# Performance work log

Hardware: AMD Instinct MI355X
Metric: run time of the kernel (lower is better)

Reference implementation:

```python
import jax, jax.numpy as jnp
import numpy as np

DIST_EPS = 0.1   # distance_eps
NORM_EPS = 0.1   # norm_eps
QUAT_EPS = 1e-3
FA_EPS = 1e-5


def normed_vec(V):
    return V / jnp.sqrt((V ** 2).sum(-1, keepdims=True) + NORM_EPS)


def collect_neighbors(node_h, edge_idx):
    # node_h: (B,N,D), edge_idx: (B,N,K) -> (B,N,K,D)
    B, N, K = edge_idx.shape
    D = node_h.shape[-1]
    idx = jnp.broadcast_to(edge_idx.reshape(B, N * K, 1), (B, N * K, D))
    return jnp.take_along_axis(node_h, idx, axis=1).reshape(B, N, K, D)


def field_average(node_h, C, num_fields):
    # per-field mean, scattered back to residues; residues with C==0 get 0
    onehot = (C[..., None] == (jnp.arange(num_fields) + 1)).astype(node_h.dtype)  # (B,N,F)
    sums = jnp.einsum('bnf,bnd->bfd', onehot, node_h)
    counts = jnp.sum(onehot, axis=1)[..., None]  # (B,F,1)
    avg = sums / (counts + FA_EPS)
    return jnp.einsum('bnf,bfd->bnd', onehot, avg)


def reference_frames(X):
    X_N, X_CA, X_C = X[:, :, 0], X[:, :, 1], X[:, :, 2]
    u_CA_N = normed_vec(X_N - X_CA)
    u_CA_C = normed_vec(X_C - X_CA)
    n_1 = u_CA_N
    n_2 = normed_vec(jnp.cross(n_1, u_CA_C))
    n_3 = normed_vec(jnp.cross(n_1, n_2))
    return jnp.stack([n_1, n_2, n_3], -1)  # (B,N,3,3), frames as columns


def reference_frames_field(X, C, num_fields):
    X_N, X_CA, X_C = X[:, :, 0], X[:, :, 1], X[:, :, 2]
    u_CA_N_avg = field_average(normed_vec(X_N - X_CA), C, num_fields)
    u_CA_C_avg = field_average(normed_vec(X_C - X_CA), C, num_fields)
    n_1 = normed_vec(u_CA_N_avg)
    n_2 = normed_vec(jnp.cross(n_1, normed_vec(u_CA_C_avg)))
    n_3 = normed_vec(jnp.cross(n_1, n_2))
    return jnp.stack([n_1, n_2, n_3], -1)


def quaternions_from_rotations(R):
    Rf = R.reshape(R.shape[:-2] + (9,))
    R00, R01, R02, R10, R11, R12, R20, R21, R22 = [Rf[..., i] for i in range(9)]
    mag = 0.5 * jnp.sqrt(jnp.abs(1.0 + jnp.stack([
        R00 + R11 + R22,
        R00 - R11 - R22,
        -R00 + R11 - R22,
        -R00 - R11 + R22], -1)) + QUAT_EPS)
    signs = jnp.sign(jnp.stack([
        jnp.ones_like(R00), R21 - R12, R02 - R20, R10 - R01], -1))
    q = signs * mag
    return q / jnp.sqrt((q ** 2).sum(-1, keepdims=True))


def transformation_features(X_i, X_j, R_i, R_j):
    dX = X_j - X_i[:, :, None]                    # (B,N,K,3)
    L = jnp.sqrt((dX ** 2).sum(-1, keepdims=True) + DIST_EPS)
    u_ij = jnp.einsum('niab,nija->nijb', R_i, dX / L)
    R_rel = jnp.einsum('niab,nijac->nijbc', R_i, R_j)
    q_ij = quaternions_from_rotations(R_rel)
    return jnp.concatenate([jnp.log(L + DIST_EPS), u_ij, q_ij], -1)  # (B,N,K,8)


def setup_inputs() -> dict:
    key = jax.random.key(0)
    k1, k2, k3 = jax.random.split(key, 3)
    B, N, K, NF = 4, 8192, 48, 16
    X = jax.random.normal(k1, (B, N, 4, 3), dtype=jnp.float32)
    edge_idx = jax.random.randint(k2, (B, N, K), 0, N).astype(jnp.int64)
    C = jax.random.randint(k3, (B, N), 0, NF + 1).astype(jnp.int64)
    return {"X": X, "edge_idx": edge_idx, "C": C, "num_fields": NF}


def reference(X, edge_idx, C, num_fields):
    B, N = X.shape[:2]
    R_i = reference_frames(X)
    R_field_i = reference_frames_field(X, C, num_fields)
    X_i = X[:, :, 1, :]  # CA
    X_j = collect_neighbors(X_i, edge_idx)
    X_field_i = field_average(X_i, C, num_fields)
    X_field_j = collect_neighbors(X_field_i, edge_idx)
    R_field_j = collect_neighbors(R_field_i.reshape(B, N, 9), edge_idx).reshape(B, N, -1, 3, 3)
    R_j = collect_neighbors(R_i.reshape(B, N, 9), edge_idx).reshape(B, N, -1, 3, 3)
    h_ff = transformation_features(X_field_i, X_field_j, R_field_i, R_field_j)
    h_fn = transformation_features(X_field_i, X_j, R_field_i, R_j)
    h_nn = transformation_features(X_i, X_j, R_i, R_j)
    edge_h = jnp.concatenate([h_ff, h_fn, h_nn], -1)  # (B,N,K,24)
    mask_i = (C > 0).astype(edge_h.dtype)[..., None]  # (B,N,1)
    mask_j = collect_neighbors(mask_i, edge_idx)      # (B,N,K,1)
    mask_ij = mask_i[:, :, None] * mask_j
    return mask_ij * edge_h
```

## Files before the change

### kernel.cpp

```cpp
#include <hip/hip_runtime.h>
#include <math.h>

#define NFIELDS 16
#define BATCH   4
#define R64_STRIDE 10

#define DIST_EPS 0.1
#define NORM_EPS 0.1
#define QUAT_EPS 0.001
#define FA_EPS   1e-5

#define TAU_NN 1e-4f
#define TAU_FN 1e-5f

#define FS_THREADS 256
__global__ void prep_pass(const float* __restrict__ X, const int* __restrict__ C,
                          double* __restrict__ Rws64, float* __restrict__ nodeF2,
                          double* __restrict__ accum,
                          int N, int BN, int nodeBlocks) {
    __shared__ double red[FS_THREADS][10];
    int t = threadIdx.x;

    if ((int)blockIdx.x < nodeBlocks) {
        int bn = blockIdx.x * blockDim.x + t;
        if (bn >= BN) return;
        const float* xp = X + (size_t)bn * 12;
        double ax = xp[3], ay = xp[4], az = xp[5];

        double ux = (double)xp[0] - ax, uy = (double)xp[1] - ay, uz = (double)xp[2] - az;
        double r1 = 1.0 / sqrt(ux * ux + uy * uy + uz * uz + NORM_EPS);
        ux *= r1; uy *= r1; uz *= r1;

        double vx = (double)xp[6] - ax, vy = (double)xp[7] - ay, vz = (double)xp[8] - az;
        double r2 = 1.0 / sqrt(vx * vx + vy * vy + vz * vz + NORM_EPS);
        vx *= r2; vy *= r2; vz *= r2;

        double wx = uy * vz - uz * vy, wy = uz * vx - ux * vz, wz = ux * vy - uy * vx;
        double r3 = 1.0 / sqrt(wx * wx + wy * wy + wz * wz + NORM_EPS);
        wx *= r3; wy *= r3; wz *= r3;

        double px = uy * wz - uz * wy, py = uz * wx - ux * wz, pz = ux * wy - uy * wx;
        double r4 = 1.0 / sqrt(px * px + py * py + pz * pz + NORM_EPS);
        px *= r4; py *= r4; pz *= r4;

        double* R = Rws64 + (size_t)bn * R64_STRIDE;
        R[0] = ux; R[1] = uy; R[2] = uz;
        R[3] = wx; R[4] = wy; R[5] = wz;
        R[6] = px; R[7] = py; R[8] = pz;

        int c = C[bn];
        float4* nf = (float4*)(nodeF2 + (size_t)bn * 16);
        nf[0] = make_float4((float)ux, (float)uy, (float)uz, (float)wx);
        nf[1] = make_float4((float)wy, (float)wz, (float)px, (float)py);
        nf[2] = make_float4((float)pz, xp[3], xp[4], xp[5]);
        nf[3] = make_float4((float)c, 0.f, 0.f, 0.f);
        return;
    }

    int fb = blockIdx.x - nodeBlocks;
    int b  = fb / NFIELDS;
    int f  = fb % NFIELDS + 1;
    const float* Xb = X + (size_t)b * N * 12;
    const int*   Cb = C + (size_t)b * N;

    double s[10];
#pragma unroll
    for (int i = 0; i < 10; i++) s[i] = 0.0;

    for (int n = t; n < N; n += FS_THREADS) {
        if (Cb[n] == f) {
            const float* xp = Xb + (size_t)n * 12;
            double ax = xp[3], ay = xp[4], az = xp[5];
            double ux = (double)xp[0] - ax, uy = (double)xp[1] - ay, uz = (double)xp[2] - az;
            double r1 = 1.0 / sqrt(ux * ux + uy * uy + uz * uz + NORM_EPS);
            double vx = (double)xp[6] - ax, vy = (double)xp[7] - ay, vz = (double)xp[8] - az;
            double r2 = 1.0 / sqrt(vx * vx + vy * vy + vz * vz + NORM_EPS);
            s[0] += ux * r1; s[1] += uy * r1; s[2] += uz * r1;
            s[3] += vx * r2; s[4] += vy * r2; s[5] += vz * r2;
            s[6] += ax;      s[7] += ay;      s[8] += az;
            s[9] += 1.0;
        }
    }

#pragma unroll
    for (int i = 0; i < 10; i++) red[t][i] = s[i];
    __syncthreads();
    for (int off = FS_THREADS / 2; off > 0; off >>= 1) {
        if (t < off) {
#pragma unroll
            for (int i = 0; i < 10; i++) red[t][i] += red[t + off][i];
        }
        __syncthreads();
    }
    if (t < 10) accum[(size_t)fb * 10 + t] = red[0][t];
}

__device__ __forceinline__ double sgn64(double x) {
    return x > 0.0 ? 1.0 : (x < 0.0 ? -1.0 : 0.0);
}

__device__ __forceinline__ void tf64(double xix, double xiy, double xiz,
                                     double xjx, double xjy, double xjz,
                                     const double* __restrict__ Ri,
                                     const double* __restrict__ Rj,
                                     float* __restrict__ o) {
    double dx = xjx - xix, dy = xjy - xiy, dz = xjz - xiz;
    double L = sqrt(dx * dx + dy * dy + dz * dz + DIST_EPS);
    o[0] = (float)log(L + DIST_EPS);
    double il = 1.0 / L;
    double vx = dx * il, vy = dy * il, vz = dz * il;
    o[1] = (float)(Ri[0] * vx + Ri[1] * vy + Ri[2] * vz);
    o[2] = (float)(Ri[3] * vx + Ri[4] * vy + Ri[5] * vz);
    o[3] = (float)(Ri[6] * vx + Ri[7] * vy + Ri[8] * vz);

    double r00 = Ri[0] * Rj[0] + Ri[1] * Rj[1] + Ri[2] * Rj[2];
    double r01 = Ri[0] * Rj[3] + Ri[1] * Rj[4] + Ri[2] * Rj[5];
    double r02 = Ri[0] * Rj[6] + Ri[1] * Rj[7] + Ri[2] * Rj[8];
    double r10 = Ri[3] * Rj[0] + Ri[4] * Rj[1] + Ri[5] * Rj[2];
    double r11 = Ri[3] * Rj[3] + Ri[4] * Rj[4] + Ri[5] * Rj[5];
    double r12 = Ri[3] * Rj[6] + Ri[4] * Rj[7] + Ri[5] * Rj[8];
    double r20 = Ri[6] * Rj[0] + Ri[7] * Rj[1] + Ri[8] * Rj[2];
    double r21 = Ri[6] * Rj[3] + Ri[7] * Rj[4] + Ri[8] * Rj[5];
    double r22 = Ri[6] * Rj[6] + Ri[7] * Rj[7] + Ri[8] * Rj[8];

    double m0 = 0.5 * sqrt(fabs(1.0 + r00 + r11 + r22) + QUAT_EPS);
    double m1 = 0.5 * sqrt(fabs(1.0 + r00 - r11 - r22) + QUAT_EPS);
    double m2 = 0.5 * sqrt(fabs(1.0 - r00 + r11 - r22) + QUAT_EPS);
    double m3 = 0.5 * sqrt(fabs(1.0 - r00 - r11 + r22) + QUAT_EPS);
    double q0 = m0;
    double q1 = sgn64(r21 - r12) * m1;
    double q2 = sgn64(r02 - r20) * m2;
    double q3 = sgn64(r10 - r01) * m3;
    double qn = 1.0 / sqrt(q0 * q0 + q1 * q1 + q2 * q2 + q3 * q3);
    o[4] = (float)(q0 * qn); o[5] = (float)(q1 * qn);
    o[6] = (float)(q2 * qn); o[7] = (float)(q3 * qn);
}

__global__ void field_finish(const double* __restrict__ accum,
                             double* __restrict__ table64,
                             float* __restrict__ tableF,
                             float* __restrict__ hff) {
    int b = blockIdx.x;
    int t = threadIdx.x;

    if (t <= NFIELDS) {
        double* e = table64 + ((size_t)b * (NFIELDS + 1) + t) * 12;
        float*  eF = tableF + ((size_t)b * (NFIELDS + 1) + t) * 12;
        if (t == 0) {
#pragma unroll
            for (int i = 0; i < 12; i++) { e[i] = 0.0; eF[i] = 0.f; }
        } else {
            const double* s = accum + (size_t)(b * NFIELDS + t - 1) * 10;
            double inv = 1.0 / (s[9] + FA_EPS);
            double axv = s[0] * inv, ayv = s[1] * inv, azv = s[2] * inv;
            double bxv = s[3] * inv, byv = s[4] * inv, bzv = s[5] * inv;
            double xx  = s[6] * inv, xy  = s[7] * inv, xz  = s[8] * inv;

            double r1 = 1.0 / sqrt(axv * axv + ayv * ayv + azv * azv + NORM_EPS);
            double n1x = axv * r1, n1y = ayv * r1, n1z = azv * r1;
            double r2 = 1.0 / sqrt(bxv * bxv + byv * byv + bzv * bzv + NORM_EPS);
            bxv *= r2; byv *= r2; bzv *= r2;

            double wx = n1y * bzv - n1z * byv, wy = n1z * bxv - n1x * bzv, wz = n1x * byv - n1y * bxv;
            double r3 = 1.0 / sqrt(wx * wx + wy * wy + wz * wz + NORM_EPS);
            wx *= r3; wy *= r3; wz *= r3;

            double px = n1y * wz - n1z * wy, py = n1z * wx - n1x * wz, pz = n1x * wy - n1y * wx;
            double r4 = 1.0 / sqrt(px * px + py * py + pz * pz + NORM_EPS);
            px *= r4; py *= r4; pz *= r4;

            e[0] = n1x; e[1] = n1y; e[2] = n1z;
            e[3] = wx;  e[4] = wy;  e[5] = wz;
            e[6] = px;  e[7] = py;  e[8] = pz;
            e[9] = xx;  e[10] = xy; e[11] = xz;
#pragma unroll
            for (int i = 0; i < 12; i++) eF[i] = (float)e[i];
        }
    }
    __syncthreads();

    int ci = t >> 4, cj = t & 15;
    const double* fi = table64 + ((size_t)b * (NFIELDS + 1) + ci + 1) * 12;
    const double* fj = table64 + ((size_t)b * (NFIELDS + 1) + cj + 1) * 12;
    float o[8];
    tf64(fi[9], fi[10], fi[11], fj[9], fj[10], fj[11], fi, fj, o);
    float* hp = hff + (((size_t)b * NFIELDS + ci) * NFIELDS + cj) * 8;
    ((float4*)hp)[0] = make_float4(o[0], o[1], o[2], o[3]);
    ((float4*)hp)[1] = make_float4(o[4], o[5], o[6], o[7]);
}

__device__ __forceinline__ void tf32(float xix, float xiy, float xiz,
                                     float xjx, float xjy, float xjz,
                                     const float* __restrict__ Ri,
                                     const float* __restrict__ Rj,
                                     float s1, float s2, float s3,
                                     float* __restrict__ o) {
    float dx = xjx - xix, dy = xjy - xiy, dz = xjz - xiz;
    float L = sqrtf(dx * dx + dy * dy + dz * dz + 0.1f);
    o[0] = logf(L + 0.1f);
    float il = 1.f / L;
    float vx = dx * il, vy = dy * il, vz = dz * il;
    o[1] = Ri[0] * vx + Ri[1] * vy + Ri[2] * vz;
    o[2] = Ri[3] * vx + Ri[4] * vy + Ri[5] * vz;
    o[3] = Ri[6] * vx + Ri[7] * vy + Ri[8] * vz;

    float r00 = Ri[0] * Rj[0] + Ri[1] * Rj[1] + Ri[2] * Rj[2];
    float r11 = Ri[3] * Rj[3] + Ri[4] * Rj[4] + Ri[5] * Rj[5];
    float r22 = Ri[6] * Rj[6] + Ri[7] * Rj[7] + Ri[8] * Rj[8];

    float m0 = 0.5f * sqrtf(fabsf(1.f + r00 + r11 + r22) + 0.001f);
    float m1 = 0.5f * sqrtf(fabsf(1.f + r00 - r11 - r22) + 0.001f);
    float m2 = 0.5f * sqrtf(fabsf(1.f - r00 + r11 - r22) + 0.001f);
    float m3 = 0.5f * sqrtf(fabsf(1.f - r00 - r11 + r22) + 0.001f);
    float q0 = m0;
    float q1 = s1 * m1;
    float q2 = s2 * m2;
    float q3 = s3 * m3;
    float qn = rsqrtf(q0 * q0 + q1 * q1 + q2 * q2 + q3 * q3);
    o[4] = q0 * qn; o[5] = q1 * qn; o[6] = q2 * qn; o[7] = q3 * qn;
}

__device__ __forceinline__ float fsgn(float x) {
    return x > 0.f ? 1.f : (x < 0.f ? -1.f : 0.f);
}
__device__ __forceinline__ float fsgnd(double x) {
    return x > 0.0 ? 1.f : (x < 0.0 ? -1.f : 0.f);
}
__device__ __forceinline__ int hswz(int idx16) {
    return idx16 ^ ((idx16 >> 3) & 7);
}

__device__ __forceinline__ void edge_core(
        float4 j0, float4 j1, float4 j2, float4 i0, float4 i1, float4 i2,
        const float* __restrict__ tableF, const double* __restrict__ Rws64,
        const double* __restrict__ table64,
        int b, int bn, int bj, int cn, float* __restrict__ o) {
    const float4* ftp = (const float4*)(tableF + ((size_t)b * (NFIELDS + 1) + cn) * 12);
    float4 f0 = ftp[0], f1 = ftp[1], f2 = ftp[2];

    float rj[9] = { j0.x, j0.y, j0.z, j0.w, j1.x, j1.y, j1.z, j1.w, j2.x };
    float cjx = j2.y, cjy = j2.z, cjz = j2.w;
    float ri[9] = { i0.x, i0.y, i0.z, i0.w, i1.x, i1.y, i1.z, i1.w, i2.x };
    float cix = i2.y, ciy = i2.z, ciz = i2.w;
    float fF[9] = { f0.x, f0.y, f0.z, f0.w, f1.x, f1.y, f1.z, f1.w, f2.x };
    float fpx = f2.y, fpy = f2.z, fpz = f2.w;

    float a21 = ri[6]*rj[3] + ri[7]*rj[4] + ri[8]*rj[5] - (ri[3]*rj[6] + ri[4]*rj[7] + ri[5]*rj[8]);
    float a02 = ri[0]*rj[6] + ri[1]*rj[7] + ri[2]*rj[8] - (ri[6]*rj[0] + ri[7]*rj[1] + ri[8]*rj[2]);
    float a10 = ri[3]*rj[0] + ri[4]*rj[1] + ri[5]*rj[2] - (ri[0]*rj[3] + ri[1]*rj[4] + ri[2]*rj[5]);
    float g21 = fF[6]*rj[3] + fF[7]*rj[4] + fF[8]*rj[5] - (fF[3]*rj[6] + fF[4]*rj[7] + fF[5]*rj[8]);
    float g02 = fF[0]*rj[6] + fF[1]*rj[7] + fF[2]*rj[8] - (fF[6]*rj[0] + fF[7]*rj[1] + fF[8]*rj[2]);
    float g10 = fF[3]*rj[0] + fF[4]*rj[1] + fF[5]*rj[2] - (fF[0]*rj[3] + fF[1]*rj[4] + fF[2]*rj[5]);

    float sa21 = fsgn(a21), sa02 = fsgn(a02), sa10 = fsgn(a10);
    float sg21 = fsgn(g21), sg02 = fsgn(g02), sg10 = fsgn(g10);

    float amin = fminf(fminf(fabsf(a21), fabsf(a02)), fabsf(a10));
    float gmin = fminf(fminf(fabsf(g21), fabsf(g02)), fabsf(g10));
    if (amin < TAU_NN || gmin < TAU_FN) {
        const double* RJ = Rws64 + (size_t)bj * R64_STRIDE;
        const double* RI = Rws64 + (size_t)bn * R64_STRIDE;
        const double* FD = table64 + ((size_t)b * (NFIELDS + 1) + cn) * 12;
        double d21 = RI[6]*RJ[3] + RI[7]*RJ[4] + RI[8]*RJ[5] - (RI[3]*RJ[6] + RI[4]*RJ[7] + RI[5]*RJ[8]);
        double d02 = RI[0]*RJ[6] + RI[1]*RJ[7] + RI[2]*RJ[8] - (RI[6]*RJ[0] + RI[7]*RJ[1] + RI[8]*RJ[2]);
        double d10 = RI[3]*RJ[0] + RI[4]*RJ[1] + RI[5]*RJ[2] - (RI[0]*RJ[3] + RI[1]*RJ[4] + RI[2]*RJ[5]);
        double e21 = FD[6]*RJ[3] + FD[7]*RJ[4] + FD[8]*RJ[5] - (FD[3]*RJ[6] + FD[4]*RJ[7] + FD[5]*RJ[8]);
        double e02 = FD[0]*RJ[6] + FD[1]*RJ[7] + FD[2]*RJ[8] - (FD[6]*RJ[0] + FD[7]*RJ[1] + FD[8]*RJ[2]);
        double e10 = FD[3]*RJ[0] + FD[4]*RJ[1] + FD[5]*RJ[2] - (FD[0]*RJ[3] + FD[1]*RJ[4] + FD[2]*RJ[5]);
        sa21 = fsgnd(d21); sa02 = fsgnd(d02); sa10 = fsgnd(d10);
        sg21 = fsgnd(e21); sg02 = fsgnd(e02); sg10 = fsgnd(e10);
    }

    tf32(fpx, fpy, fpz, cjx, cjy, cjz, fF, rj, sg21, sg02, sg10, o + 8);
    tf32(cix, ciy, ciz, cjx, cjy, cjz, ri, rj, sa21, sa02, sa10, o + 16);
}

template <int KC, int NC>
__global__ __launch_bounds__(256)
void edge_pass_lds(const float* __restrict__ nodeF2, const int* __restrict__ eidx,
                   const float* __restrict__ tableF, const float* __restrict__ hff,
                   const double* __restrict__ Rws64, const double* __restrict__ table64,
                   float* __restrict__ out) {
    __shared__ float4 s_hff[2 * NFIELDS * NFIELDS];
    __shared__ float  s_st[128 * 28];

    const int t   = threadIdx.x;
    const int tid = blockIdx.x * 256 + t;
    const int b   = tid / (KC * NC);
    const int bn  = tid / KC;
    const int bj  = b * NC + eidx[tid];

    {
        const float4* src = (const float4*)(hff + (size_t)b * (NFIELDS * NFIELDS * 8));
        s_hff[hswz(t)]       = src[t];
        s_hff[hswz(t + 256)] = src[t + 256];
    }

    const float4* rjp = (const float4*)(nodeF2 + (size_t)bj * 16);
    float4 j0 = rjp[0], j1 = rjp[1], j2 = rjp[2], j3 = rjp[3];
    const float4* rip = (const float4*)(nodeF2 + (size_t)bn * 16);
    float4 i0 = rip[0], i1 = rip[1], i2 = rip[2], i3 = rip[3];

    const int cj = (int)j3.x;
    const int cn = (int)i3.x;
    const bool valid = (cn > 0) && (cj > 0);

    float o[24];
    if (valid) {
        edge_core(j0, j1, j2, i0, i1, i2, tableF, Rws64, table64, b, bn, bj, cn, o);
    } else {
#pragma unroll
        for (int i = 8; i < 24; i++) o[i] = 0.f;
    }

    __syncthreads();
    if (valid) {
        int e = ((cn - 1) * NFIELDS + (cj - 1)) * 2;
        float4 h0 = s_hff[hswz(e)];
        float4 h1 = s_hff[hswz(e + 1)];
        o[0] = h0.x; o[1] = h0.y; o[2] = h0.z; o[3] = h0.w;
        o[4] = h1.x; o[5] = h1.y; o[6] = h1.z; o[7] = h1.w;
    } else {
#pragma unroll
        for (int i = 0; i < 8; i++) o[i] = 0.f;
    }

    float4* outv = (float4*)out + (size_t)blockIdx.x * 1536;

    if (t < 128) {
#pragma unroll
        for (int c = 0; c < 6; c++)
            *(float4*)(s_st + t * 28 + c * 4) =
                make_float4(o[4*c], o[4*c+1], o[4*c+2], o[4*c+3]);
    }
    __syncthreads();
#pragma unroll
    for (int r = 0; r < 3; r++) {
        int f  = t + 256 * r;
        int el = f / 6, c = f - el * 6;
        outv[f] = *(const float4*)(s_st + el * 28 + c * 4);
    }
    __syncthreads();
    if (t >= 128) {
#pragma unroll
        for (int c = 0; c < 6; c++)
            *(float4*)(s_st + (t - 128) * 28 + c * 4) =
                make_float4(o[4*c], o[4*c+1], o[4*c+2], o[4*c+3]);
    }
    __syncthreads();
#pragma unroll
    for (int r = 0; r < 3; r++) {
        int f  = 768 + t + 256 * r;
        int fe = f / 6;
        int el = fe - 128, c = f - fe * 6;
        outv[f] = *(const float4*)(s_st + el * 28 + c * 4);
    }
}

__global__ void edge_pass_gen(const float* __restrict__ nodeF2,
                              const int* __restrict__ eidx,
                              const float* __restrict__ tableF,
                              const float* __restrict__ hff,
                              const double* __restrict__ Rws64,
                              const double* __restrict__ table64,
                              float* __restrict__ out,
                              int N, int K, int total) {
    int tid = blockIdx.x * blockDim.x + threadIdx.x;
    if (tid >= total) return;
    int bn = tid / K;
    int b  = bn / N;
    int bj = b * N + eidx[tid];

    const float4* rjp = (const float4*)(nodeF2 + (size_t)bj * 16);
    float4 j0 = rjp[0], j1 = rjp[1], j2 = rjp[2], j3 = rjp[3];
    const float4* rip = (const float4*)(nodeF2 + (size_t)bn * 16);
    float4 i0 = rip[0], i1 = rip[1], i2 = rip[2], i3 = rip[3];
    int cj = (int)j3.x;
    int cn = (int)i3.x;

    float o[24];
    if (cn > 0 && cj > 0) {
        const float4* hp = (const float4*)(hff +
            (((size_t)b * NFIELDS + (cn - 1)) * NFIELDS + (cj - 1)) * 8);
        float4 h0 = hp[0], h1 = hp[1];
        o[0] = h0.x; o[1] = h0.y; o[2] = h0.z; o[3] = h0.w;
        o[4] = h1.x; o[5] = h1.y; o[6] = h1.z; o[7] = h1.w;
        edge_core(j0, j1, j2, i0, i1, i2, tableF, Rws64, table64, b, bn, bj, cn, o);
    } else {
#pragma unroll
        for (int i = 0; i < 24; i++) o[i] = 0.f;
    }

    float4* op = (float4*)(out + (size_t)tid * 24);
#pragma unroll
    for (int i = 0; i < 6; i++)
        op[i] = make_float4(o[4 * i], o[4 * i + 1], o[4 * i + 2], o[4 * i + 3]);
}

extern "C" void kernel_launch(void* const* d_in, const int* in_sizes, int n_in,
                              void* d_out, int out_size, void* d_ws, size_t ws_size,
                              hipStream_t stream) {
    const float* X  = (const float*)d_in[0];
    const int* eidx = (const int*)d_in[1];
    const int* C    = (const int*)d_in[2];

    const int B  = BATCH;
    const int BN = in_sizes[2];
    const int N  = BN / B;
    const int total = in_sizes[1];
    const int K  = total / BN;

    double* accum   = (double*)d_ws;
    double* table64 = accum + B * NFIELDS * 10;
    double* Rws64   = table64 + B * (NFIELDS + 1) * 12;
    float*  nodeF2  = (float*)(Rws64 + (size_t)BN * R64_STRIDE);
    float*  tableF  = nodeF2 + (size_t)BN * 16;
    float*  hff     = tableF + B * (NFIELDS + 1) * 12;

    int nodeBlocks = (BN + 255) / 256;
    prep_pass<<<nodeBlocks + B * NFIELDS, FS_THREADS, 0, stream>>>(
        X, C, Rws64, nodeF2, accum, N, BN, nodeBlocks);
    field_finish<<<B, 256, 0, stream>>>(accum, table64, tableF, hff);

    if (K == 48 && N == 8192 && (total % 256) == 0) {
        edge_pass_lds<48, 8192><<<total / 256, 256, 0, stream>>>(
            nodeF2, eidx, tableF, hff, Rws64, table64, (float*)d_out);
    } else {
        int eb = (total + 255) / 256;
        edge_pass_gen<<<eb, 256, 0, stream>>>(nodeF2, eidx, tableF, hff,
                                              Rws64, table64, (float*)d_out,
                                              N, K, total);
    }
}
```

Before: 72.85 us.

## Compress node records to 48 bytes, recompute third frame axis, stage field table in LDS

Each per-node record now drops the stored third frame vector and is packed into three float4s instead of four. Edge threads rebuild n3 from n1 and n2 with a cross product and rsqrt, which cuts gather traffic per edge. The per-field frame table is loaded once per block into shared memory instead of being fetched from global per edge. The float-sign fallback thresholds are tightened so the double-precision path triggers less often, trading some sign-robustness margin for fewer slow-path loads, and the recomputed n3 carries a small float error.

```diff
diff --git a/kernel.cpp b/kernel.cpp
--- a/kernel.cpp
+++ b/kernel.cpp
@@ -10,8 +10,8 @@
 #define QUAT_EPS 0.001
 #define FA_EPS   1e-5
 
-#define TAU_NN 1e-4f
-#define TAU_FN 1e-5f
+#define TAU_NN 2e-5f
+#define TAU_FN 2e-6f
 
 #define FS_THREADS 256
 __global__ void prep_pass(const float* __restrict__ X, const int* __restrict__ C,
@@ -51,9 +51,8 @@
         int c = C[bn];
         float4* nf = (float4*)(nodeF2 + (size_t)bn * 16);
         nf[0] = make_float4((float)ux, (float)uy, (float)uz, (float)wx);
-        nf[1] = make_float4((float)wy, (float)wz, (float)px, (float)py);
-        nf[2] = make_float4((float)pz, xp[3], xp[4], xp[5]);
-        nf[3] = make_float4((float)c, 0.f, 0.f, 0.f);
+        nf[1] = make_float4((float)wy, (float)wz, xp[3], xp[4]);
+        nf[2] = make_float4(xp[5], (float)c, 0.f, 0.f);
         return;
     }
 
@@ -229,22 +228,21 @@
 __device__ __forceinline__ int hswz(int idx16) {
     return idx16 ^ ((idx16 >> 3) & 7);
 }
+__device__ __forceinline__ void n3_recompute(const float* __restrict__ r ,
+                                             float* __restrict__ n3) {
+    float px = r[1] * r[5] - r[2] * r[4];
+    float py = r[2] * r[3] - r[0] * r[5];
+    float pz = r[0] * r[4] - r[1] * r[3];
+    float rr = rsqrtf(px * px + py * py + pz * pz + 0.1f);
+    n3[0] = px * rr; n3[1] = py * rr; n3[2] = pz * rr;
+}
 
 __device__ __forceinline__ void edge_core(
-        float4 j0, float4 j1, float4 j2, float4 i0, float4 i1, float4 i2,
-        const float* __restrict__ tableF, const double* __restrict__ Rws64,
-        const double* __restrict__ table64,
+        const float* __restrict__ rj, const float* __restrict__ cjp,
+        const float* __restrict__ ri, const float* __restrict__ cip,
+        const float* __restrict__ fF, const float* __restrict__ fp,
+        const double* __restrict__ Rws64, const double* __restrict__ table64,
         int b, int bn, int bj, int cn, float* __restrict__ o) {
-    const float4* ftp = (const float4*)(tableF + ((size_t)b * (NFIELDS + 1) + cn) * 12);
-    float4 f0 = ftp[0], f1 = ftp[1], f2 = ftp[2];
-
-    float rj[9] = { j0.x, j0.y, j0.z, j0.w, j1.x, j1.y, j1.z, j1.w, j2.x };
-    float cjx = j2.y, cjy = j2.z, cjz = j2.w;
-    float ri[9] = { i0.x, i0.y, i0.z, i0.w, i1.x, i1.y, i1.z, i1.w, i2.x };
-    float cix = i2.y, ciy = i2.z, ciz = i2.w;
-    float fF[9] = { f0.x, f0.y, f0.z, f0.w, f1.x, f1.y, f1.z, f1.w, f2.x };
-    float fpx = f2.y, fpy = f2.z, fpz = f2.w;
-
     float a21 = ri[6]*rj[3] + ri[7]*rj[4] + ri[8]*rj[5] - (ri[3]*rj[6] + ri[4]*rj[7] + ri[5]*rj[8]);
     float a02 = ri[0]*rj[6] + ri[1]*rj[7] + ri[2]*rj[8] - (ri[6]*rj[0] + ri[7]*rj[1] + ri[8]*rj[2]);
     float a10 = ri[3]*rj[0] + ri[4]*rj[1] + ri[5]*rj[2] - (ri[0]*rj[3] + ri[1]*rj[4] + ri[2]*rj[5]);
@@ -271,8 +269,8 @@
         sg21 = fsgnd(e21); sg02 = fsgnd(e02); sg10 = fsgnd(e10);
     }
 
-    tf32(fpx, fpy, fpz, cjx, cjy, cjz, fF, rj, sg21, sg02, sg10, o + 8);
-    tf32(cix, ciy, ciz, cjx, cjy, cjz, ri, rj, sa21, sa02, sa10, o + 16);
+    tf32(fp[0], fp[1], fp[2], cjp[0], cjp[1], cjp[2], fF, rj, sg21, sg02, sg10, o + 8);
+    tf32(cip[0], cip[1], cip[2], cjp[0], cjp[1], cjp[2], ri, rj, sa21, sa02, sa10, o + 16);
 }
 
 template <int KC, int NC>
@@ -282,6 +280,7 @@
                    const double* __restrict__ Rws64, const double* __restrict__ table64,
                    float* __restrict__ out) {
     __shared__ float4 s_hff[2 * NFIELDS * NFIELDS];
+    __shared__ float4 s_tf[(NFIELDS + 1) * 3];
     __shared__ float  s_st[128 * 28];
 
     const int t   = threadIdx.x;
@@ -294,27 +293,38 @@
         const float4* src = (const float4*)(hff + (size_t)b * (NFIELDS * NFIELDS * 8));
         s_hff[hswz(t)]       = src[t];
         s_hff[hswz(t + 256)] = src[t + 256];
+        if (t < (NFIELDS + 1) * 3)
+            s_tf[t] = ((const float4*)(tableF + (size_t)b * (NFIELDS + 1) * 12))[t];
     }
 
     const float4* rjp = (const float4*)(nodeF2 + (size_t)bj * 16);
-    float4 j0 = rjp[0], j1 = rjp[1], j2 = rjp[2], j3 = rjp[3];
+    float4 j0 = rjp[0], j1 = rjp[1], j2 = rjp[2];
     const float4* rip = (const float4*)(nodeF2 + (size_t)bn * 16);
-    float4 i0 = rip[0], i1 = rip[1], i2 = rip[2], i3 = rip[3];
-
-    const int cj = (int)j3.x;
-    const int cn = (int)i3.x;
+    float4 i0 = rip[0], i1 = rip[1], i2 = rip[2];
+
+    const int cj = (int)j2.y;
+    const int cn = (int)i2.y;
     const bool valid = (cn > 0) && (cj > 0);
+
+    float rj[9] = { j0.x, j0.y, j0.z, j0.w, j1.x, j1.y, 0, 0, 0 };
+    float cjp[3] = { j1.z, j1.w, j2.x };
+    float ri[9] = { i0.x, i0.y, i0.z, i0.w, i1.x, i1.y, 0, 0, 0 };
+    float cip[3] = { i1.z, i1.w, i2.x };
+    n3_recompute(rj, rj + 6);
+    n3_recompute(ri, ri + 6);
+
+    __syncthreads();
 
     float o[24];
     if (valid) {
-        edge_core(j0, j1, j2, i0, i1, i2, tableF, Rws64, table64, b, bn, bj, cn, o);
-    } else {
-#pragma unroll
-        for (int i = 8; i < 24; i++) o[i] = 0.f;
-    }
-
-    __syncthreads();
-    if (valid) {
+        float fF[9], fp[3];
+        float4 f0 = s_tf[cn * 3 + 0], f1 = s_tf[cn * 3 + 1], f2 = s_tf[cn * 3 + 2];
+        fF[0] = f0.x; fF[1] = f0.y; fF[2] = f0.z; fF[3] = f0.w;
+        fF[4] = f1.x; fF[5] = f1.y; fF[6] = f1.z; fF[7] = f1.w;
+        fF[8] = f2.x; fp[0] = f2.y; fp[1] = f2.z; fp[2] = f2.w;
+
+        edge_core(rj, cjp, ri, cip, fF, fp, Rws64, table64, b, bn, bj, cn, o);
+
         int e = ((cn - 1) * NFIELDS + (cj - 1)) * 2;
         float4 h0 = s_hff[hswz(e)];
         float4 h1 = s_hff[hswz(e + 1)];
@@ -322,7 +332,7 @@
         o[4] = h1.x; o[5] = h1.y; o[6] = h1.z; o[7] = h1.w;
     } else {
 #pragma unroll
-        for (int i = 0; i < 8; i++) o[i] = 0.f;
+        for (int i = 0; i < 24; i++) o[i] = 0.f;
     }
 
     float4* outv = (float4*)out + (size_t)blockIdx.x * 1536;
@@ -372,20 +382,32 @@
     int bj = b * N + eidx[tid];
 
     const float4* rjp = (const float4*)(nodeF2 + (size_t)bj * 16);
-    float4 j0 = rjp[0], j1 = rjp[1], j2 = rjp[2], j3 = rjp[3];
+    float4 j0 = rjp[0], j1 = rjp[1], j2 = rjp[2];
     const float4* rip = (const float4*)(nodeF2 + (size_t)bn * 16);
-    float4 i0 = rip[0], i1 = rip[1], i2 = rip[2], i3 = rip[3];
-    int cj = (int)j3.x;
-    int cn = (int)i3.x;
+    float4 i0 = rip[0], i1 = rip[1], i2 = rip[2];
+    int cj = (int)j2.y;
+    int cn = (int)i2.y;
 
     float o[24];
     if (cn > 0 && cj > 0) {
+        float rj[9] = { j0.x, j0.y, j0.z, j0.w, j1.x, j1.y, 0, 0, 0 };
+        float cjp[3] = { j1.z, j1.w, j2.x };
+        float ri[9] = { i0.x, i0.y, i0.z, i0.w, i1.x, i1.y, 0, 0, 0 };
+        float cip[3] = { i1.z, i1.w, i2.x };
+        n3_recompute(rj, rj + 6);
+        n3_recompute(ri, ri + 6);
+
+        const float4* ftp = (const float4*)(tableF + ((size_t)b * (NFIELDS + 1) + cn) * 12);
+        float4 f0 = ftp[0], f1 = ftp[1], f2 = ftp[2];
+        float fF[9] = { f0.x, f0.y, f0.z, f0.w, f1.x, f1.y, f1.z, f1.w, f2.x };
+        float fp[3] = { f2.y, f2.z, f2.w };
+
         const float4* hp = (const float4*)(hff +
             (((size_t)b * NFIELDS + (cn - 1)) * NFIELDS + (cj - 1)) * 8);
         float4 h0 = hp[0], h1 = hp[1];
         o[0] = h0.x; o[1] = h0.y; o[2] = h0.z; o[3] = h0.w;
         o[4] = h1.x; o[5] = h1.y; o[6] = h1.z; o[7] = h1.w;
-        edge_core(j0, j1, j2, i0, i1, i2, tableF, Rws64, table64, b, bn, bj, cn, o);
+        edge_core(rj, cjp, ri, cip, fF, fp, Rws64, table64, b, bn, bj, cn, o);
     } else {
 #pragma unroll
         for (int i = 0; i < 24; i++) o[i] = 0.f;
```

Result: faster. 69.34 us (-4.8%).
